# Kernel tuning notes

Measured on AMD Instinct MI355X. Metric: run time of the kernel, lower is better.

## Reference

```python
import jax, jax.numpy as jnp
import numpy as np

N = 200000      # nodes
C = 256         # scalar channels
VC = 16         # vector channels
VD = 3          # vector spatial dim
M = 50000       # number of motifs (segments)


def setup_inputs() -> dict:
    key = jax.random.key(0)
    ks, kv, kb, kw1, kb1, kw2, kb2 = jax.random.split(key, 7)
    s = jax.random.normal(ks, (N, C), dtype=jnp.float32)
    v = jax.random.normal(kv, (N, VC, VD), dtype=jnp.float32)
    motif_batch = jax.random.randint(kb, (N,), 0, M, dtype=jnp.int64)
    # Linear(channels, channels)
    Ws = jax.random.normal(kw1, (C, C), dtype=jnp.float32) / np.sqrt(C)
    bs = jax.random.normal(kb1, (C,), dtype=jnp.float32) * 0.01
    # Linear(16, 16)
    Wv = jax.random.normal(kw2, (VC, VC), dtype=jnp.float32) / np.sqrt(VC)
    bv = jax.random.normal(kb2, (VC,), dtype=jnp.float32) * 0.01
    return {"s": s, "v": v, "motif_batch": motif_batch,
            "Ws": Ws, "bs": bs, "Wv": Wv, "bv": bv}


def _scatter_mean(x, seg, num_segments):
    # robust scatter mean: sum / max(count, 1)
    sums = jax.ops.segment_sum(x, seg, num_segments=num_segments)
    cnt = jax.ops.segment_sum(jnp.ones((x.shape[0],), x.dtype), seg,
                              num_segments=num_segments)
    cnt = jnp.maximum(cnt, 1.0)
    return sums / cnt.reshape((num_segments,) + (1,) * (x.ndim - 1))


def reference(s, v, motif_batch, Ws, bs, Wv, bv):
    seg = motif_batch.reshape(-1)
    s_motif = _scatter_mean(s, seg, M)            # [M, C]
    v_motif = _scatter_mean(v, seg, M)            # [M, VC, VD]
    s_out = s_motif @ Ws.T + bs                   # [M, C]
    # v_pool(v_motif.transpose(1,2)).transpose(1,2):
    # Linear over the VC axis, spatial dim untouched
    v_out = jnp.einsum('mcd,oc->mod', v_motif, Wv) + bv[None, :, None]
    return (s_out, v_out)
```

## Files before the change

kernel.cpp:

```cpp
#include <hip/hip_runtime.h>

#define N_NODES 200000
#define C 256
#define VC 16
#define VD 3
#define VDIM (VC * VD)
#define M_MOTIFS 50000
#define M_PAD 50048
#define CAP 64

#define NODE_BLOCKS ((N_NODES + 255) / 256)
#define CVT_BLOCKS  ((C * C) / (256 * 4))
#define GATHER_BLOCKS (M_MOTIFS / 4)
#define GEMM_BLOCKS 512
#define NTILES (M_PAD / 64)

typedef __attribute__((ext_vector_type(8))) __bf16 bf16x8;
typedef __attribute__((ext_vector_type(4))) float f32x4;

__device__ __forceinline__ unsigned short f2bf(float x) {
  unsigned u = __builtin_bit_cast(unsigned, x);
  u += 0x7fffu + ((u >> 16) & 1u);
  return (unsigned short)(u >> 16);
}

__global__ __launch_bounds__(256) void fill_kernel(
    const int* __restrict__ seg, int* __restrict__ cnt,
    int* __restrict__ nodelist, const float* __restrict__ Ws,
    unsigned short* __restrict__ Wsb) {
  int b = blockIdx.x, t = threadIdx.x;
  if (b < NODE_BLOCKS) {
    int i = b * 256 + t;
    if (i < N_NODES) {
      int m = seg[i];
      int r = atomicAdd(&cnt[m], 1);
      if (r < CAP) nodelist[(size_t)m * CAP + r] = i;
    }
  } else {
    int i = ((b - NODE_BLOCKS) * 256 + t) * 4;
    float4 w = *(const float4*)(Ws + i);
    ushort4 o;
    o.x = f2bf(w.x); o.y = f2bf(w.y); o.z = f2bf(w.z); o.w = f2bf(w.w);
    *(ushort4*)(Wsb + i) = o;
  }
}

__global__ __launch_bounds__(256) void gather_kernel(
    const float* __restrict__ s, const float* __restrict__ v,
    const int* __restrict__ cnt, const int* __restrict__ nodelist,
    const float* __restrict__ Wv, const float* __restrict__ bv,
    unsigned short* __restrict__ s_motif, float* __restrict__ v_out) {
  int m = (blockIdx.x * 256 + threadIdx.x) >> 6;
  int lane = threadIdx.x & 63;

  int k = cnt[m];
  int idv = nodelist[(size_t)m * CAP + (lane & 15)];

  if (k == 0) {
    ushort4 z; z.x = z.y = z.z = z.w = 0;
    ((ushort4*)(s_motif + (size_t)m * C))[lane] = z;
    if (lane < VDIM) v_out[(size_t)m * VDIM + lane] = bv[lane / 3];
    return;
  }

  int km1 = k - 1;
  int kc = min(k, CAP);

  int i0 = __shfl(idv, 0, 64);
  int i1 = __shfl(idv, min(1, km1), 64);
  int i2 = __shfl(idv, min(2, km1), 64);
  int i3 = __shfl(idv, min(3, km1), 64);
  float4 a0 = ((const float4*)(s + (size_t)i0 * C))[lane];
  float4 a1 = ((const float4*)(s + (size_t)i1 * C))[lane];
  float4 a2 = ((const float4*)(s + (size_t)i2 * C))[lane];
  float4 a3 = ((const float4*)(s + (size_t)i3 * C))[lane];
  float vb0 = 0.f, vb1 = 0.f, vb2 = 0.f, vb3 = 0.f;
  if (lane < VDIM) {
    vb0 = v[(size_t)i0 * VDIM + lane];
    vb1 = v[(size_t)i1 * VDIM + lane];
    vb2 = v[(size_t)i2 * VDIM + lane];
    vb3 = v[(size_t)i3 * VDIM + lane];
  }
  float4 acc = a0;
  float vacc = vb0;
  if (k > 1) { acc.x += a1.x; acc.y += a1.y; acc.z += a1.z; acc.w += a1.w; vacc += vb1; }
  if (k > 2) { acc.x += a2.x; acc.y += a2.y; acc.z += a2.z; acc.w += a2.w; vacc += vb2; }
  if (k > 3) { acc.x += a3.x; acc.y += a3.y; acc.z += a3.z; acc.w += a3.w; vacc += vb3; }

  if (k > 4) {
    int i4 = __shfl(idv, min(4, km1), 64);
    int i5 = __shfl(idv, min(5, km1), 64);
    int i6 = __shfl(idv, min(6, km1), 64);
    int i7 = __shfl(idv, min(7, km1), 64);
    float4 b4 = ((const float4*)(s + (size_t)i4 * C))[lane];
    float4 b5 = ((const float4*)(s + (size_t)i5 * C))[lane];
    float4 b6 = ((const float4*)(s + (size_t)i6 * C))[lane];
    float4 b7 = ((const float4*)(s + (size_t)i7 * C))[lane];
    float w4 = 0.f, w5 = 0.f, w6 = 0.f, w7 = 0.f;
    if (lane < VDIM) {
      w4 = v[(size_t)i4 * VDIM + lane];
      w5 = v[(size_t)i5 * VDIM + lane];
      w6 = v[(size_t)i6 * VDIM + lane];
      w7 = v[(size_t)i7 * VDIM + lane];
    }
    acc.x += b4.x; acc.y += b4.y; acc.z += b4.z; acc.w += b4.w; vacc += w4;
    if (k > 5) { acc.x += b5.x; acc.y += b5.y; acc.z += b5.z; acc.w += b5.w; vacc += w5; }
    if (k > 6) { acc.x += b6.x; acc.y += b6.y; acc.z += b6.z; acc.w += b6.w; vacc += w6; }
    if (k > 7) { acc.x += b7.x; acc.y += b7.y; acc.z += b7.z; acc.w += b7.w; vacc += w7; }
  }

  if (k > 8) {
    int idv2 = nodelist[(size_t)m * CAP + lane];
    for (int j = 8; j < kc; ++j) {
      int ij = __shfl(idv2, j, 64);
      float4 a = ((const float4*)(s + (size_t)ij * C))[lane];
      acc.x += a.x; acc.y += a.y; acc.z += a.z; acc.w += a.w;
      if (lane < VDIM) vacc += v[(size_t)ij * VDIM + lane];
    }
  }

  float rc = 1.0f / (float)k;
  ushort4 o;
  o.x = f2bf(acc.x * rc); o.y = f2bf(acc.y * rc);
  o.z = f2bf(acc.z * rc); o.w = f2bf(acc.w * rc);
  ((ushort4*)(s_motif + (size_t)m * C))[lane] = o;

  float vm = vacc * rc;
  if (lane < VDIM) {
    int oo = lane / 3, d = lane - oo * 3;
    float vo = bv[oo];
#pragma unroll
    for (int c2 = 0; c2 < VC; ++c2)
      vo += Wv[oo * VC + c2] * __shfl(vm, c2 * 3 + d, 64);
    v_out[(size_t)m * VDIM + lane] = vo;
  }
}

__global__ __launch_bounds__(256, 2) void gemm_persistB_kernel(
    const unsigned short* __restrict__ A16,
    const unsigned short* __restrict__ B16,
    const float* __restrict__ bs, float* __restrict__ out) {
  __shared__ unsigned short Bs[128 * 256];
  int tid = threadIdx.x;
  int half = blockIdx.x & 1;
  int bstart = blockIdx.x >> 1;
  int n0 = half * 128;

#pragma unroll
  for (int it = 0; it < 16; ++it) {
    int chunk = it * 256 + tid;
    int row = chunk >> 5, cpos = chunk & 31;
    bf16x8 w = *(const bf16x8*)(B16 + (size_t)(n0 + row) * C + cpos * 8);
    int byte = row * 512 + ((cpos * 16) ^ ((row & 7) << 4));
    *(bf16x8*)((char*)Bs + byte) = w;
  }
  __syncthreads();

  int wave = tid >> 6, lane = tid & 63;
  int rl = lane & 15;
  int quad = lane >> 4;
  int kq = quad * 8;
  int rq = quad * 4;

  float bias[8];
#pragma unroll
  for (int j = 0; j < 8; ++j) bias[j] = bs[n0 + j * 16 + rl];

  for (int t = bstart; t < NTILES; t += 256) {
    int m0 = t * 64;
    int mrow = m0 + wave * 16 + rl;
    const unsigned short* Ab = A16 + (size_t)mrow * C + kq;
    bf16x8 af[8];
#pragma unroll
    for (int kk = 0; kk < 8; ++kk)
      af[kk] = *(const bf16x8*)(Ab + kk * 32);

    f32x4 acc[8] = {};
#pragma unroll
    for (int kk = 0; kk < 8; ++kk) {
#pragma unroll
      for (int j = 0; j < 8; ++j) {
        int rowl = j * 16 + rl;
        int byte = rowl * 512 + ((kk * 64 + quad * 16) ^ ((rowl & 7) << 4));
        bf16x8 bf = *(const bf16x8*)((const char*)Bs + byte);
        acc[j] = __builtin_amdgcn_mfma_f32_16x16x32_bf16(af[kk], bf, acc[j],
                                                         0, 0, 0);
      }
    }

#pragma unroll
    for (int j = 0; j < 8; ++j) {
      int cn = n0 + j * 16 + rl;
#pragma unroll
      for (int r = 0; r < 4; ++r) {
        int gm = m0 + wave * 16 + rq + r;
        if (gm < M_MOTIFS) out[(size_t)gm * C + cn] = acc[j][r] + bias[j];
      }
    }
  }
}

extern "C" void kernel_launch(void* const* d_in, const int* in_sizes, int n_in,
                              void* d_out, int out_size, void* d_ws, size_t ws_size,
                              hipStream_t stream) {
  const float* s  = (const float*)d_in[0];
  const float* v  = (const float*)d_in[1];
  const int*   seg = (const int*)d_in[2];
  const float* Ws = (const float*)d_in[3];
  const float* bs = (const float*)d_in[4];
  const float* Wv = (const float*)d_in[5];
  const float* bv = (const float*)d_in[6];

  float* out   = (float*)d_out;
  float* s_out = out;
  float* v_out = out + (size_t)M_MOTIFS * C;

  int* cnt      = (int*)d_ws;
  int* nodelist = cnt + M_MOTIFS;
  unsigned short* Wsb     = (unsigned short*)(nodelist + (size_t)M_MOTIFS * CAP);
  unsigned short* s_motif = Wsb + (size_t)C * C;

  hipMemsetAsync(cnt, 0, M_MOTIFS * sizeof(int), stream);
  fill_kernel<<<NODE_BLOCKS + CVT_BLOCKS, 256, 0, stream>>>(seg, cnt, nodelist,
                                                            Ws, Wsb);
  gather_kernel<<<GATHER_BLOCKS, 256, 0, stream>>>(s, v, cnt, nodelist, Wv, bv,
                                                   s_motif, v_out);
  gemm_persistB_kernel<<<GEMM_BLOCKS, 256, 0, stream>>>(s_motif, Wsb, bs, s_out);
}
```

Baseline: 127.7 us.

## Hold GEMM weight fragments in registers instead of LDS, per-wave N split

The GEMM kernel stops staging half of the bf16 weight matrix in shared memory. Each wave instead keeps its 64-column slice of B for all of K in registers, and each block processes 16-row M tiles across all 256 output columns. This removes the LDS fill, the barrier and the per-MFMA LDS reads. The cost is much higher register pressure (128 VGPRs for B alone) and each A row tile being loaded by all four waves. Separately, the gather kernel now skips the nodelist load for empty motifs.

```diff
diff --git a/kernel.cpp b/kernel.cpp
--- a/kernel.cpp
+++ b/kernel.cpp
@@ -6,14 +6,13 @@
 #define VD 3
 #define VDIM (VC * VD)
 #define M_MOTIFS 50000
-#define M_PAD 50048
 #define CAP 64
 
 #define NODE_BLOCKS ((N_NODES + 255) / 256)
 #define CVT_BLOCKS  ((C * C) / (256 * 4))
 #define GATHER_BLOCKS (M_MOTIFS / 4)
 #define GEMM_BLOCKS 512
-#define NTILES (M_PAD / 64)
+#define NTILES (M_MOTIFS / 16)
 
 typedef __attribute__((ext_vector_type(8))) __bf16 bf16x8;
 typedef __attribute__((ext_vector_type(4))) float f32x4;
@@ -52,9 +51,7 @@
     unsigned short* __restrict__ s_motif, float* __restrict__ v_out) {
   int m = (blockIdx.x * 256 + threadIdx.x) >> 6;
   int lane = threadIdx.x & 63;
-
   int k = cnt[m];
-  int idv = nodelist[(size_t)m * CAP + (lane & 15)];
 
   if (k == 0) {
     ushort4 z; z.x = z.y = z.z = z.w = 0;
@@ -63,6 +60,7 @@
     return;
   }
 
+  int idv = nodelist[(size_t)m * CAP + (lane & 15)];
   int km1 = k - 1;
   int kc = min(k, CAP);
 
@@ -136,66 +134,52 @@
   }
 }
 
-__global__ __launch_bounds__(256, 2) void gemm_persistB_kernel(
+__global__ __launch_bounds__(256, 2) void gemm_regB_kernel(
     const unsigned short* __restrict__ A16,
     const unsigned short* __restrict__ B16,
     const float* __restrict__ bs, float* __restrict__ out) {
-  __shared__ unsigned short Bs[128 * 256];
   int tid = threadIdx.x;
-  int half = blockIdx.x & 1;
-  int bstart = blockIdx.x >> 1;
-  int n0 = half * 128;
-
-#pragma unroll
-  for (int it = 0; it < 16; ++it) {
-    int chunk = it * 256 + tid;
-    int row = chunk >> 5, cpos = chunk & 31;
-    bf16x8 w = *(const bf16x8*)(B16 + (size_t)(n0 + row) * C + cpos * 8);
-    int byte = row * 512 + ((cpos * 16) ^ ((row & 7) << 4));
-    *(bf16x8*)((char*)Bs + byte) = w;
-  }
-  __syncthreads();
-
   int wave = tid >> 6, lane = tid & 63;
+  int wn0 = wave * 64;
   int rl = lane & 15;
   int quad = lane >> 4;
   int kq = quad * 8;
   int rq = quad * 4;
 
-  float bias[8];
-#pragma unroll
-  for (int j = 0; j < 8; ++j) bias[j] = bs[n0 + j * 16 + rl];
-
-  for (int t = bstart; t < NTILES; t += 256) {
-    int m0 = t * 64;
-    int mrow = m0 + wave * 16 + rl;
-    const unsigned short* Ab = A16 + (size_t)mrow * C + kq;
+  const unsigned short* Bb = B16 + (size_t)(wn0 + rl) * C + kq;
+  bf16x8 bf[8][4];
+#pragma unroll
+  for (int kk = 0; kk < 8; ++kk)
+#pragma unroll
+    for (int j = 0; j < 4; ++j)
+      bf[kk][j] = *(const bf16x8*)(Bb + (size_t)j * 16 * C + kk * 32);
+
+  float bias[4];
+#pragma unroll
+  for (int j = 0; j < 4; ++j) bias[j] = bs[wn0 + j * 16 + rl];
+
+  for (int t = blockIdx.x; t < NTILES; t += GEMM_BLOCKS) {
+    int m0 = t * 16;
+    const unsigned short* Ab = A16 + (size_t)(m0 + rl) * C + kq;
     bf16x8 af[8];
 #pragma unroll
     for (int kk = 0; kk < 8; ++kk)
       af[kk] = *(const bf16x8*)(Ab + kk * 32);
 
-    f32x4 acc[8] = {};
-#pragma unroll
-    for (int kk = 0; kk < 8; ++kk) {
-#pragma unroll
-      for (int j = 0; j < 8; ++j) {
-        int rowl = j * 16 + rl;
-        int byte = rowl * 512 + ((kk * 64 + quad * 16) ^ ((rowl & 7) << 4));
-        bf16x8 bf = *(const bf16x8*)((const char*)Bs + byte);
-        acc[j] = __builtin_amdgcn_mfma_f32_16x16x32_bf16(af[kk], bf, acc[j],
-                                                         0, 0, 0);
-      }
-    }
-
-#pragma unroll
-    for (int j = 0; j < 8; ++j) {
-      int cn = n0 + j * 16 + rl;
-#pragma unroll
-      for (int r = 0; r < 4; ++r) {
-        int gm = m0 + wave * 16 + rq + r;
-        if (gm < M_MOTIFS) out[(size_t)gm * C + cn] = acc[j][r] + bias[j];
-      }
+    f32x4 acc[4] = {};
+#pragma unroll
+    for (int kk = 0; kk < 8; ++kk)
+#pragma unroll
+      for (int j = 0; j < 4; ++j)
+        acc[j] = __builtin_amdgcn_mfma_f32_16x16x32_bf16(af[kk], bf[kk][j],
+                                                         acc[j], 0, 0, 0);
+
+#pragma unroll
+    for (int j = 0; j < 4; ++j) {
+      int cn = wn0 + j * 16 + rl;
+#pragma unroll
+      for (int r = 0; r < 4; ++r)
+        out[(size_t)(m0 + rq + r) * C + cn] = acc[j][r] + bias[j];
     }
   }
 }
@@ -225,5 +209,5 @@
                                                             Ws, Wsb);
   gather_kernel<<<GATHER_BLOCKS, 256, 0, stream>>>(s, v, cnt, nodelist, Wv, bv,
                                                    s_motif, v_out);
-  gemm_persistB_kernel<<<GEMM_BLOCKS, 256, 0, stream>>>(s_motif, Wsb, bs, s_out);
-}
+  gemm_regB_kernel<<<GEMM_BLOCKS, 256, 0, stream>>>(s_motif, Wsb, bs, s_out);
+}
```

Result: faster. 108.1 us (-15.3%).
